# Kernel optimization log

Measured on AMD Instinct MI355X. Metric: run time of the kernel, lower is better.

Reference implementation:

```python
import jax, jax.numpy as jnp
import numpy as np

L = 48.0      # cubic box edge
DL = 4.0      # k-grid spacing param -> nk = int(L/DL) = 12
N = 8192      # atoms
D = 128       # feature channels
TWOPI = 2.0 * np.pi


def _k_index_sets():
    """Replicates torch mask.nonzero() ordering and the (k_vectors - 1) index
    shift of compute_potential_optimized. The shifted indices are remapped to
    effective integer exponents (torch negative indexing wraps, i.e. modulo)."""
    nk = int(L / DL)
    kx = np.arange(nk + 1)
    ky = np.arange(-nk, nk + 1)
    kz = np.arange(-nk, nk + 1)
    KX, KY, KZ = np.meshgrid(kx, ky, kz, indexing='ij')
    ksq = KX.astype(np.float64) ** 2 + KY ** 2 + KZ ** 2
    mask = (ksq <= (L / DL) ** 2) & (ksq > 0)
    ix, iy, iz = np.nonzero(mask)  # row-major, same order as torch .nonzero()
    # forward potential: value[:, :, ix-1, iy-1, iz-1] with wraparound ->
    # effective exponents via modulo of the per-axis table sizes
    ex = (ix - 1) % (nk + 1)                      # eikx col c -> exponent c
    ey = ((iy - 1) % (2 * nk + 1)) - nk           # eiky col c -> exponent c-nk
    ez = ((iz - 1) % (2 * nk + 1)) - nk
    k_fwd = np.stack([ex, ey, ez], axis=1).astype(np.int32)
    # inverse transform: unshifted valid k-vectors, negative sign in exponent
    k_inv = np.stack([ix, iy - nk, iz - nk], axis=1).astype(np.int32)
    return k_fwd, k_inv


def setup_inputs() -> dict:
    key = jax.random.key(0)
    kq, kk, kv, kr = jax.random.split(key, 4)
    k_fwd, k_inv = _k_index_sets()
    cell = jnp.eye(3, dtype=jnp.float32)[None] * jnp.float32(L)  # [1,3,3]
    return {
        'q_vector': jax.random.normal(kq, (N, D), dtype=jnp.float32),
        'k_vector': jax.random.normal(kk, (N, D), dtype=jnp.float32),
        'v_vector': jax.random.normal(kv, (N, D), dtype=jnp.float32),
        'positions': jax.random.uniform(kr, (N, 3), dtype=jnp.float32) * jnp.float32(L),
        'cell': cell,
        'batch': jnp.zeros((N,), dtype=jnp.int64),
        'k_fwd': jnp.asarray(k_fwd),
        'k_inv': jnp.asarray(k_inv),
    }


def reference(q_vector, k_vector, v_vector, positions, cell, batch, k_fwd, k_inv):
    # single batch (batch is all zeros); box = diagonal of the cell
    box = jnp.diagonal(cell.reshape(-1, 3, 3), axis1=-2, axis2=-1)[0]  # [3]
    rfrac = positions / box                                            # [n,3]
    # plane waves at the selected k-vectors; |eik| == 1
    phase_f = TWOPI * (rfrac @ k_fwd.T.astype(rfrac.dtype))            # [n,K]
    eik_f = jnp.exp(1j * phase_f)                                      # complex64
    phase_i = TWOPI * (rfrac @ k_inv.T.astype(rfrac.dtype))
    eik_i = jnp.exp(-1j * phase_i)                                     # [n,K]
    cdt = eik_f.dtype
    # k/v potentials: structure-factor sums over atoms -> [K,d]
    k_pot = jnp.einsum('nk,nd->kd', eik_f, k_vector.astype(cdt))
    v_pot = jnp.einsum('nk,nd->kd', eik_f, v_vector.astype(cdt))
    # |q_pot[n,d,k]| = |q[n,d]|*|eik[n,k]| = |q[n,d]| exactly, so the einsum
    # 'ijk,jk->ij' over abs values collapses to a real GEMM:
    aw = jnp.abs(q_vector) @ jnp.abs(k_pot).T                          # [n,K]
    # max-shift + log_softmax + exp == softmax over the k axis
    sm = jax.nn.softmax(aw, axis=-1)
    # inverse transform fused: sum_k sm[n,k]*eik_i[n,k]*v_pot[k,d]
    out = jnp.real(jnp.einsum('nk,kd->nd', sm.astype(cdt) * eik_i, v_pot))
    return out
```

## Files before the change

kernel.cpp:

```cpp
#include <hip/hip_runtime.h>
#include <hip/hip_bf16.h>

#define D128 128
#define NSPLIT 8
#define KT 64
#define SNR 32
#define SKT 128
#define TOPS 8
#define FCAP 16

typedef float4 f4;
typedef __attribute__((ext_vector_type(8))) short short8v;
typedef __attribute__((ext_vector_type(4))) float f32x4;

__device__ __forceinline__ unsigned short f2bu(float x){
  __hip_bfloat16 h = __float2bfloat16(x);
  return *(unsigned short*)&h;
}
__device__ __forceinline__ float bu2f(unsigned short u){
  return __uint_as_float(((unsigned)u) << 16);
}

#define GLDS16(gp, lp) __builtin_amdgcn_global_load_lds( \
    (const __attribute__((address_space(1))) unsigned int*)(const void*)(gp), \
    (__attribute__((address_space(3))) unsigned int*)(lp), 16, 0, 0)

__global__ __launch_bounds__(256) void k_zero(float* __restrict__ p, int total){
  int i = blockIdx.x*256 + threadIdx.x;
  int stride = gridDim.x*256;
  for(; i < total; i += stride) p[i] = 0.f;
}

__global__ __launch_bounds__(256) void k_cvt(const float* __restrict__ pos,
    const float* __restrict__ cell, float* __restrict__ rfrac,
    const float* __restrict__ q, const float* __restrict__ kvec,
    const float* __restrict__ vvec, unsigned short* __restrict__ kvhT,
    unsigned short* __restrict__ kvlT, unsigned short* __restrict__ vvhT,
    unsigned short* __restrict__ qa_bf, int N){
  __shared__ float sk[32][132], sv[32][132];
  const int tid = threadIdx.x;
  const int c0 = blockIdx.x*32;
  if(tid < 32){
    int i = c0 + tid;
    float bx = cell[0], by = cell[4], bz = cell[8];
    f4 r; r.x = pos[i*3+0]/bx; r.y = pos[i*3+1]/by; r.z = pos[i*3+2]/bz; r.w = 0.f;
    ((f4*)rfrac)[i] = r;
  }
  #pragma unroll
  for(int i=0;i<2;i++){
    int idx = tid + i*256;
    int row = idx >> 4, c = idx & 15;
    const float* src = q + (size_t)(c0+row)*D128 + c*8;
    f4 v0 = *(const f4*)src, v1 = *(const f4*)(src+4);
    uint4 o;
    o.x = (unsigned)f2bu(fabsf(v0.x)) | ((unsigned)f2bu(fabsf(v0.y))<<16);
    o.y = (unsigned)f2bu(fabsf(v0.z)) | ((unsigned)f2bu(fabsf(v0.w))<<16);
    o.z = (unsigned)f2bu(fabsf(v1.x)) | ((unsigned)f2bu(fabsf(v1.y))<<16);
    o.w = (unsigned)f2bu(fabsf(v1.z)) | ((unsigned)f2bu(fabsf(v1.w))<<16);
    *(uint4*)(qa_bf + (size_t)(c0+row)*D128 + ((c ^ (row&7))<<3)) = o;
  }
  #pragma unroll
  for(int i=0;i<4;i++){
    int idx = tid + i*256;
    int a = idx >> 5, fq = idx & 31;
    f4 v = ((const f4*)(kvec + (size_t)(c0+a)*D128))[fq];
    *(f4*)&sk[a][fq*4] = v;
    f4 u = ((const f4*)(vvec + (size_t)(c0+a)*D128))[fq];
    *(f4*)&sv[a][fq*4] = u;
  }
  __syncthreads();
  #pragma unroll
  for(int i=0;i<4;i++){
    int idx = tid + i*256;
    int d = idx >> 3, aq = idx & 7;
    size_t ob = (size_t)d*N + c0 + aq*4;
    ushort4 h, l, vh;
    float x0 = sk[aq*4+0][d], x1 = sk[aq*4+1][d], x2 = sk[aq*4+2][d], x3 = sk[aq*4+3][d];
    h.x = f2bu(x0); h.y = f2bu(x1); h.z = f2bu(x2); h.w = f2bu(x3);
    l.x = f2bu(x0 - bu2f(h.x)); l.y = f2bu(x1 - bu2f(h.y));
    l.z = f2bu(x2 - bu2f(h.z)); l.w = f2bu(x3 - bu2f(h.w));
    vh.x = f2bu(sv[aq*4+0][d]); vh.y = f2bu(sv[aq*4+1][d]);
    vh.z = f2bu(sv[aq*4+2][d]); vh.w = f2bu(sv[aq*4+3][d]);
    *(ushort4*)(kvhT + ob) = h;
    *(ushort4*)(kvlT + ob) = l;
    *(ushort4*)(vvhT + ob) = vh;
  }
}

__global__ __launch_bounds__(512) void k_pot_mfma(
    const unsigned short* __restrict__ kvhT, const unsigned short* __restrict__ kvlT,
    const unsigned short* __restrict__ vvhT, const float* __restrict__ rfrac,
    const int* __restrict__ kfwd, float* __restrict__ pot4, int N, int K){
  const int tid = threadIdx.x;
  const int k0 = blockIdx.x*KT;
  const int split = blockIdx.y;
  const int part = N/NSPLIT;
  const int abase = split*part;
  __shared__ unsigned short Ae[2][4][KT][32];
  __shared__ unsigned short Bl[2][3][D128][32];
  const int w = tid >> 6, l = tid & 63, l15 = l & 15, g = l >> 4;
  const int kp = tid >> 4;
  const int a0 = (tid & 15)*2;
  float kfa[2][3];
  {
    int r0 = min(k0 + kp*2,     K-1);
    int r1 = min(k0 + kp*2 + 1, K-1);
    kfa[0][0] = (float)kfwd[3*r0]; kfa[0][1] = (float)kfwd[3*r0+1]; kfa[0][2] = (float)kfwd[3*r0+2];
    kfa[1][0] = (float)kfwd[3*r1]; kfa[1][1] = (float)kfwd[3*r1+1]; kfa[1][2] = (float)kfwd[3*r1+2];
  }
  f32x4 acc[4][4];
  #pragma unroll
  for(int i=0;i<4;i++)
    #pragma unroll
    for(int j=0;j<4;j++)
      acc[i][j] = (f32x4){0.f,0.f,0.f,0.f};
  const int rowS = w*16 + (l >> 2);
  const int csrc = (((l & 3) ^ ((l >> 3) & 3)))*8;
  const int cA   = (g ^ ((l15 >> 1) & 3))*8;

  auto stage = [&](int buf, int c0a){
    size_t goff = (size_t)rowS*N + c0a + csrc;
    GLDS16(kvhT + goff, &Bl[buf][0][w*16][0]);
    GLDS16(kvlT + goff, &Bl[buf][1][w*16][0]);
    GLDS16(vvhT + goff, &Bl[buf][2][w*16][0]);
  };
  auto egen = [&](int buf, int c0a){
    f4 r0 = ((const f4*)rfrac)[c0a + a0];
    f4 r1 = ((const f4*)rfrac)[c0a + a0 + 1];
    #pragma unroll
    for(int kk=0; kk<2; kk++){
      int kloc = kp*2 + kk;
      float t0 = __builtin_amdgcn_fractf(r0.x*kfa[kk][0] + r0.y*kfa[kk][1] + r0.z*kfa[kk][2]);
      float t1 = __builtin_amdgcn_fractf(r1.x*kfa[kk][0] + r1.y*kfa[kk][1] + r1.z*kfa[kk][2]);
      float c0v = __builtin_amdgcn_cosf(t0), s0v = __builtin_amdgcn_sinf(t0);
      float c1v = __builtin_amdgcn_cosf(t1), s1v = __builtin_amdgcn_sinf(t1);
      unsigned cb0 = __float_as_uint(c0v), cb1 = __float_as_uint(c1v);
      unsigned sb0 = __float_as_uint(s0v), sb1 = __float_as_uint(s1v);
      unsigned chp = (cb0 >> 16) | (cb1 & 0xffff0000u);
      unsigned shp = (sb0 >> 16) | (sb1 & 0xffff0000u);
      float cl0 = c0v - __uint_as_float(cb0 & 0xffff0000u);
      float cl1 = c1v - __uint_as_float(cb1 & 0xffff0000u);
      float sl0 = s0v - __uint_as_float(sb0 & 0xffff0000u);
      float sl1 = s1v - __uint_as_float(sb1 & 0xffff0000u);
      unsigned clp = (unsigned)f2bu(cl0) | ((unsigned)f2bu(cl1) << 16);
      unsigned slp = (unsigned)f2bu(sl0) | ((unsigned)f2bu(sl1) << 16);
      int off = (((a0>>3) ^ ((kloc>>1)&3)) << 3) | (a0 & 7);
      *(unsigned*)&Ae[buf][0][kloc][off] = chp;
      *(unsigned*)&Ae[buf][1][kloc][off] = clp;
      *(unsigned*)&Ae[buf][2][kloc][off] = shp;
      *(unsigned*)&Ae[buf][3][kloc][off] = slp;
    }
  };

  stage(0, abase); egen(0, abase);
  __syncthreads();
  const int nch = part/32;
  for(int ch=0; ch<nch; ch++){
    int cur = ch & 1;
    if(ch+1 < nch){ stage(cur^1, abase + (ch+1)*32); egen(cur^1, abase + (ch+1)*32); }
    short8v bKh = *(const short8v*)&Bl[cur][0][w*16 + l15][cA];
    short8v bKl = *(const short8v*)&Bl[cur][1][w*16 + l15][cA];
    short8v bVh = *(const short8v*)&Bl[cur][2][w*16 + l15][cA];
    #pragma unroll
    for(int ks=0; ks<4; ks++){
      short8v e0 = *(const short8v*)&Ae[cur][0][ks*16 + l15][cA];
      short8v e1 = *(const short8v*)&Ae[cur][1][ks*16 + l15][cA];
      short8v e2 = *(const short8v*)&Ae[cur][2][ks*16 + l15][cA];
      short8v e3 = *(const short8v*)&Ae[cur][3][ks*16 + l15][cA];
      acc[ks][0] = __builtin_amdgcn_mfma_f32_16x16x32_bf16(e0, bKh, acc[ks][0], 0,0,0);
      acc[ks][1] = __builtin_amdgcn_mfma_f32_16x16x32_bf16(e2, bKh, acc[ks][1], 0,0,0);
      acc[ks][2] = __builtin_amdgcn_mfma_f32_16x16x32_bf16(e0, bVh, acc[ks][2], 0,0,0);
      acc[ks][3] = __builtin_amdgcn_mfma_f32_16x16x32_bf16(e2, bVh, acc[ks][3], 0,0,0);
      acc[ks][0] = __builtin_amdgcn_mfma_f32_16x16x32_bf16(e0, bKl, acc[ks][0], 0,0,0);
      acc[ks][1] = __builtin_amdgcn_mfma_f32_16x16x32_bf16(e2, bKl, acc[ks][1], 0,0,0);
      acc[ks][0] = __builtin_amdgcn_mfma_f32_16x16x32_bf16(e1, bKh, acc[ks][0], 0,0,0);
      acc[ks][1] = __builtin_amdgcn_mfma_f32_16x16x32_bf16(e3, bKh, acc[ks][1], 0,0,0);
    }
    __syncthreads();
  }
  size_t M = (size_t)K*D128;
  #pragma unroll
  for(int ks=0; ks<4; ks++){
    #pragma unroll
    for(int reg=0; reg<4; reg++){
      int k = k0 + ks*16 + g*4 + reg;
      if(k < K){
        int d = w*16 + l15;
        size_t base = (size_t)k*D128 + d;
        atomicAdd(&pot4[base],       acc[ks][0][reg]);
        atomicAdd(&pot4[base + M],   acc[ks][1][reg]);
        atomicAdd(&pot4[base + 2*M], acc[ks][2][reg]);
        atomicAdd(&pot4[base + 3*M], acc[ks][3][reg]);
      }
    }
  }
}

__global__ __launch_bounds__(256) void k_merge(const float* __restrict__ pot4,
    float* __restrict__ kabs, unsigned short* __restrict__ kabs_swz,
    float* __restrict__ vcm, float* __restrict__ vsm, int K, int KPAD){
  size_t M = (size_t)K*D128;
  size_t idx = (size_t)blockIdx.x*256 + threadIdx.x;
  if(idx >= (size_t)KPAD*D128) return;
  int k = (int)(idx >> 7), d = (int)(idx & 127);
  size_t sw = (size_t)k*D128 + ((((d>>3) ^ (k&7))<<3) | (d&7));
  if(idx < M){
    float kc = pot4[idx], ks_ = pot4[M+idx], vc = pot4[2*M+idx], vs = pot4[3*M+idx];
    float ab = sqrtf(fmaf(kc,kc, ks_*ks_));
    kabs[idx] = ab;
    vcm[idx] = vc; vsm[idx] = vs;
    kabs_swz[sw] = f2bu(ab);
  } else {
    kabs_swz[sw] = 0;
  }
}

__global__ __launch_bounds__(256) void k_screen(
    const unsigned short* __restrict__ qa_bf, const unsigned short* __restrict__ kabs_swz,
    int* __restrict__ tk, float* __restrict__ taw, int N, int K, int NT){
  const int tid = threadIdx.x;
  const int w = tid >> 6, l = tid & 63, l15 = l & 15, g = l >> 4;
  const int n0 = blockIdx.x*SNR;
  const int ty = blockIdx.y;
  const int k0 = ty*SKT;
  __shared__ unsigned short Kb[SKT][D128];
  __shared__ unsigned short Qa[SNR][D128];
  __shared__ int cnt[SNR];
  __shared__ unsigned mx[SNR];
  if(tid < SNR){ cnt[tid] = 0; mx[tid] = 0u; }
  {
    int row = tid >> 3, s = tid & 7;
    size_t o = ((size_t)(n0+row)*NT + ty)*TOPS + s;
    taw[o] = -1e30f; tk[o] = -1;
  }
  #pragma unroll
  for(int j=0;j<8;j++){
    int sbase = w*512 + j*64;
    GLDS16(kabs_swz + (size_t)k0*D128 + (size_t)(sbase + l)*8,
           ((unsigned short*)Kb) + (size_t)sbase*8);
  }
  #pragma unroll
  for(int j=0;j<2;j++){
    int sbase = w*128 + j*64;
    GLDS16(qa_bf + (size_t)n0*D128 + (size_t)(sbase + l)*8,
           ((unsigned short*)Qa) + (size_t)sbase*8);
  }
  __syncthreads();
  f32x4 acc[2][2];
  #pragma unroll
  for(int i=0;i<2;i++)
    #pragma unroll
    for(int j=0;j<2;j++)
      acc[i][j] = (f32x4){0.f,0.f,0.f,0.f};
  const int sz = l15 & 7;
  #pragma unroll
  for(int ds=0; ds<4; ds++){
    int c = (((ds*4 + g) ^ sz))*8;
    short8v a0 = *(const short8v*)&Kb[w*32 + l15][c];
    short8v a1 = *(const short8v*)&Kb[w*32 + 16 + l15][c];
    short8v b0 = *(const short8v*)&Qa[l15][c];
    short8v b1 = *(const short8v*)&Qa[16 + l15][c];
    acc[0][0] = __builtin_amdgcn_mfma_f32_16x16x32_bf16(a0, b0, acc[0][0], 0,0,0);
    acc[0][1] = __builtin_amdgcn_mfma_f32_16x16x32_bf16(a0, b1, acc[0][1], 0,0,0);
    acc[1][0] = __builtin_amdgcn_mfma_f32_16x16x32_bf16(a1, b0, acc[1][0], 0,0,0);
    acc[1][1] = __builtin_amdgcn_mfma_f32_16x16x32_bf16(a1, b1, acc[1][1], 0,0,0);
  }
  #pragma unroll
  for(int jn=0; jn<2; jn++){
    float m4 = 0.f;
    #pragma unroll
    for(int ks=0; ks<2; ks++)
      #pragma unroll
      for(int r=0; r<4; r++)
        m4 = fmaxf(m4, acc[ks][jn][r]);
    atomicMax(&mx[jn*16 + l15], __float_as_uint(m4));
  }
  __syncthreads();
  #pragma unroll
  for(int jn=0; jn<2; jn++){
    int n = jn*16 + l15;
    float thr = __uint_as_float(mx[n]) - 21.0f;
    #pragma unroll
    for(int ks=0; ks<2; ks++){
      #pragma unroll
      for(int r=0; r<4; r++){
        int k = k0 + w*32 + ks*16 + g*4 + r;
        float aw = acc[ks][jn][r];
        if(k < K && aw >= thr){
          int s = atomicAdd(&cnt[n], 1);
          if(s < TOPS){
            size_t o = ((size_t)(n0+n)*NT + ty)*TOPS + s;
            taw[o] = aw; tk[o] = k;
          }
        }
      }
    }
  }
}

__global__ __launch_bounds__(256) void k_final(const float* __restrict__ q,
    const float* __restrict__ kabs, const float* __restrict__ vcm,
    const float* __restrict__ vsm, const float* __restrict__ rfrac,
    const int* __restrict__ kinv, const int* __restrict__ tk,
    const float* __restrict__ taw, float* __restrict__ out, int N, int K, int NT){
  const int rb = threadIdx.x >> 2;
  const int j  = threadIdx.x & 3;
  const int row = blockIdx.x*64 + rb;
  if(row >= N) return;
  const int NE = NT*TOPS;
  const float* trow = taw + (size_t)row*NE;
  const int*   krow = tk  + (size_t)row*NE;
  float m = -1e30f;
  for(int i=j; i<NE; i+=4) m = fmaxf(m, trow[i]);
  m = fmaxf(m, __shfl_xor(m,1)); m = fmaxf(m, __shfl_xor(m,2));
  __shared__ int lk[64][FCAP];
  __shared__ int lcnt[64];
  if(j==0) lcnt[rb] = 0;
  __syncthreads();
  for(int i=j; i<NE; i+=4){
    float aw = trow[i];
    if(aw >= m - 24.0f){
      int s = atomicAdd(&lcnt[rb], 1);
      if(s < FCAP) lk[rb][s] = krow[i];
    }
  }
  __syncthreads();
  int cn = min(lcnt[rb], FCAP);
  const float* qrow = q + (size_t)row*D128;
  float paw[FCAP];
  for(int e=0; e<cn; e++){
    int k = lk[rb][e];
    const float* ar = kabs + (size_t)k*D128;
    float p = 0.f;
    #pragma unroll
    for(int d=0; d<32; d+=4){
      int dd = j*32 + d;
      f4 qv = *(const f4*)(qrow+dd); f4 av = *(const f4*)(ar+dd);
      p = fmaf(fabsf(qv.x), av.x, p); p = fmaf(fabsf(qv.y), av.y, p);
      p = fmaf(fabsf(qv.z), av.z, p); p = fmaf(fabsf(qv.w), av.w, p);
    }
    p += __shfl_xor(p,1); p += __shfl_xor(p,2);
    paw[e] = p;
  }
  float m2 = -1e30f;
  for(int e=0;e<cn;e++) m2 = fmaxf(m2, paw[e]);
  float w[FCAP]; float Z = 0.f;
  for(int e=0;e<cn;e++){ w[e] = expf(paw[e]-m2); Z += w[e]; }
  float o[32];
  #pragma unroll
  for(int t=0;t<32;t++) o[t]=0.f;
  f4 rf = *(const f4*)(rfrac + (size_t)row*4);
  for(int e=0;e<cn;e++){
    float wn = w[e]/Z;
    if(wn < 1e-7f) continue;
    int k = lk[rb][e];
    float t = __builtin_amdgcn_fractf(rf.x*(float)kinv[k*3] + rf.y*(float)kinv[k*3+1] + rf.z*(float)kinv[k*3+2]);
    float si = __builtin_amdgcn_sinf(t), ci = __builtin_amdgcn_cosf(t);
    float wc = wn*ci, wsn = wn*si;
    const float* vcr = vcm + (size_t)k*D128 + j*32;
    const float* vsr = vsm + (size_t)k*D128 + j*32;
    #pragma unroll
    for(int d=0; d<32; d+=4){
      f4 a2 = *(const f4*)(vcr+d); f4 b2 = *(const f4*)(vsr+d);
      o[d]   = fmaf(wc, a2.x, fmaf(wsn, b2.x, o[d]));
      o[d+1] = fmaf(wc, a2.y, fmaf(wsn, b2.y, o[d+1]));
      o[d+2] = fmaf(wc, a2.z, fmaf(wsn, b2.z, o[d+2]));
      o[d+3] = fmaf(wc, a2.w, fmaf(wsn, b2.w, o[d+3]));
    }
  }
  float* orow = out + (size_t)row*D128 + j*32;
  #pragma unroll
  for(int d=0; d<32; d+=4)
    *(f4*)(orow+d) = make_float4(o[d], o[d+1], o[d+2], o[d+3]);
}

extern "C" void kernel_launch(void* const* d_in, const int* in_sizes, int n_in,
                              void* d_out, int out_size, void* d_ws, size_t ws_size,
                              hipStream_t stream){
  const float* q    = (const float*)d_in[0];
  const float* kvec = (const float*)d_in[1];
  const float* vvec = (const float*)d_in[2];
  const float* pos  = (const float*)d_in[3];
  const float* cell = (const float*)d_in[4];
  const int*   kfwd = (const int*)d_in[6];
  const int*   kinv = (const int*)d_in[7];
  const int N = in_sizes[3]/3;
  const int K = in_sizes[6]/3;
  const int NT = (K + SKT - 1)/SKT;
  const int KPAD = NT*SKT;
  const int KTILES = (K + KT - 1)/KT;

  float* ws = (float*)d_ws;
  size_t o = 0;
  float* rfrac    = ws + o; o += (size_t)N*4;
  float* pot4     = ws + o; o += (size_t)4*K*D128;
  float* kabs     = ws + o; o += (size_t)K*D128;
  float* vcm      = ws + o; o += (size_t)K*D128;
  float* vsm      = ws + o; o += (size_t)K*D128;
  unsigned short* kabs_swz = (unsigned short*)(ws + o); o += (size_t)KPAD*D128/2 + 4;
  unsigned short* qa_bf    = (unsigned short*)(ws + o); o += (size_t)N*D128/2 + 4;
  float* taw      = ws + o; o += (size_t)N*NT*TOPS;
  int*   tk       = (int*)(ws + o); o += (size_t)N*NT*TOPS;
  unsigned short* kvhT = (unsigned short*)(ws + o); o += (size_t)D128*N/2;
  unsigned short* kvlT = (unsigned short*)(ws + o); o += (size_t)D128*N/2;
  unsigned short* vvhT = (unsigned short*)(ws + o); o += (size_t)D128*N/2;
  float* out = (float*)d_out;

  k_zero<<<dim3(1024), dim3(256), 0, stream>>>(pot4, 4*K*D128);
  k_cvt<<<dim3(N/32), dim3(256), 0, stream>>>(pos, cell, rfrac, q, kvec, vvec,
      kvhT, kvlT, vvhT, qa_bf, N);
  k_pot_mfma<<<dim3(KTILES, NSPLIT), dim3(512), 0, stream>>>(
      kvhT, kvlT, vvhT, rfrac, kfwd, pot4, N, K);
  k_merge<<<dim3((KPAD*D128 + 255)/256), dim3(256), 0, stream>>>(
      pot4, kabs, kabs_swz, vcm, vsm, K, KPAD);
  k_screen<<<dim3(N/SNR, NT), dim3(256), 0, stream>>>(qa_bf, kabs_swz, tk, taw, N, K, NT);
  k_final<<<dim3((N+63)/64), dim3(256), 0, stream>>>(
      q, kabs, vcm, vsm, rfrac, kinv, tk, taw, out, N, K, NT);
}
```

Baseline: 244.8 us.

## Retile k_pot_mfma to 4 waves with 32x64 per-wave register tiles

The structure-factor MFMA kernel drops from 8 to 4 waves per block. Each wave now owns a 32(k) x 64(d) output sub-tile, so every LDS fragment of the plane-wave and feature operands is reused across more MFMAs. Plane-wave generation is reorganised so each thread computes 8 atoms for one k and writes 16-byte LDS stores instead of scattered 4-byte ones, and staging issues twice as many global-to-LDS loads per thread. The cost is many more accumulator registers per thread (128 floats) and fewer waves to hide latency.

```diff
diff --git a/kernel.cpp b/kernel.cpp
--- a/kernel.cpp
+++ b/kernel.cpp
@@ -87,7 +87,7 @@
   }
 }
 
-__global__ __launch_bounds__(512) void k_pot_mfma(
+__global__ __launch_bounds__(256) void k_pot_mfma(
     const unsigned short* __restrict__ kvhT, const unsigned short* __restrict__ kvlT,
     const unsigned short* __restrict__ vvhT, const float* __restrict__ rfrac,
     const int* __restrict__ kfwd, float* __restrict__ pot4, int N, int K){
@@ -99,57 +99,61 @@
   __shared__ unsigned short Ae[2][4][KT][32];
   __shared__ unsigned short Bl[2][3][D128][32];
   const int w = tid >> 6, l = tid & 63, l15 = l & 15, g = l >> 4;
-  const int kp = tid >> 4;
-  const int a0 = (tid & 15)*2;
-  float kfa[2][3];
+  const int kbase = (w & 1)*32, dbase = (w >> 1)*64;
+  const int ke = tid >> 2;
+  const int ae0 = (tid & 3)*8;
+  float kfx, kfy, kfz;
   {
-    int r0 = min(k0 + kp*2,     K-1);
-    int r1 = min(k0 + kp*2 + 1, K-1);
-    kfa[0][0] = (float)kfwd[3*r0]; kfa[0][1] = (float)kfwd[3*r0+1]; kfa[0][2] = (float)kfwd[3*r0+2];
-    kfa[1][0] = (float)kfwd[3*r1]; kfa[1][1] = (float)kfwd[3*r1+1]; kfa[1][2] = (float)kfwd[3*r1+2];
-  }
-  f32x4 acc[4][4];
-  #pragma unroll
-  for(int i=0;i<4;i++)
+    int kk = min(k0 + ke, K-1);
+    kfx = (float)kfwd[3*kk]; kfy = (float)kfwd[3*kk+1]; kfz = (float)kfwd[3*kk+2];
+  }
+  f32x4 acc[2][4][4];
+  #pragma unroll
+  for(int i=0;i<2;i++)
     #pragma unroll
     for(int j=0;j<4;j++)
-      acc[i][j] = (f32x4){0.f,0.f,0.f,0.f};
-  const int rowS = w*16 + (l >> 2);
-  const int csrc = (((l & 3) ^ ((l >> 3) & 3)))*8;
-  const int cA   = (g ^ ((l15 >> 1) & 3))*8;
+      #pragma unroll
+      for(int p=0;p<4;p++)
+        acc[i][j][p] = (f32x4){0.f,0.f,0.f,0.f};
+  const int csrcS = ((l & 3) ^ ((l >> 3) & 3))*8;
+  const int ccA   = (g ^ ((l15 >> 1) & 3))*8;
 
   auto stage = [&](int buf, int c0a){
-    size_t goff = (size_t)rowS*N + c0a + csrc;
-    GLDS16(kvhT + goff, &Bl[buf][0][w*16][0]);
-    GLDS16(kvlT + goff, &Bl[buf][1][w*16][0]);
-    GLDS16(vvhT + goff, &Bl[buf][2][w*16][0]);
+    #pragma unroll
+    for(int r=0; r<2; r++){
+      int rbase = r*64 + w*16;
+      size_t goff = (size_t)(rbase + (l >> 2))*N + c0a + csrcS;
+      GLDS16(kvhT + goff, &Bl[buf][0][rbase][0]);
+      GLDS16(kvlT + goff, &Bl[buf][1][rbase][0]);
+      GLDS16(vvhT + goff, &Bl[buf][2][rbase][0]);
+    }
   };
   auto egen = [&](int buf, int c0a){
-    f4 r0 = ((const f4*)rfrac)[c0a + a0];
-    f4 r1 = ((const f4*)rfrac)[c0a + a0 + 1];
-    #pragma unroll
-    for(int kk=0; kk<2; kk++){
-      int kloc = kp*2 + kk;
-      float t0 = __builtin_amdgcn_fractf(r0.x*kfa[kk][0] + r0.y*kfa[kk][1] + r0.z*kfa[kk][2]);
-      float t1 = __builtin_amdgcn_fractf(r1.x*kfa[kk][0] + r1.y*kfa[kk][1] + r1.z*kfa[kk][2]);
-      float c0v = __builtin_amdgcn_cosf(t0), s0v = __builtin_amdgcn_sinf(t0);
-      float c1v = __builtin_amdgcn_cosf(t1), s1v = __builtin_amdgcn_sinf(t1);
-      unsigned cb0 = __float_as_uint(c0v), cb1 = __float_as_uint(c1v);
-      unsigned sb0 = __float_as_uint(s0v), sb1 = __float_as_uint(s1v);
-      unsigned chp = (cb0 >> 16) | (cb1 & 0xffff0000u);
-      unsigned shp = (sb0 >> 16) | (sb1 & 0xffff0000u);
-      float cl0 = c0v - __uint_as_float(cb0 & 0xffff0000u);
-      float cl1 = c1v - __uint_as_float(cb1 & 0xffff0000u);
-      float sl0 = s0v - __uint_as_float(sb0 & 0xffff0000u);
-      float sl1 = s1v - __uint_as_float(sb1 & 0xffff0000u);
-      unsigned clp = (unsigned)f2bu(cl0) | ((unsigned)f2bu(cl1) << 16);
-      unsigned slp = (unsigned)f2bu(sl0) | ((unsigned)f2bu(sl1) << 16);
-      int off = (((a0>>3) ^ ((kloc>>1)&3)) << 3) | (a0 & 7);
-      *(unsigned*)&Ae[buf][0][kloc][off] = chp;
-      *(unsigned*)&Ae[buf][1][kloc][off] = clp;
-      *(unsigned*)&Ae[buf][2][kloc][off] = shp;
-      *(unsigned*)&Ae[buf][3][kloc][off] = slp;
-    }
+    unsigned ow0[4], ow1[4], ow2[4], ow3[4];
+    #pragma unroll
+    for(int jp=0; jp<4; jp++){
+      f4 ra = ((const f4*)rfrac)[c0a + ae0 + jp*2];
+      f4 rb = ((const f4*)rfrac)[c0a + ae0 + jp*2 + 1];
+      float ta = __builtin_amdgcn_fractf(ra.x*kfx + ra.y*kfy + ra.z*kfz);
+      float tb = __builtin_amdgcn_fractf(rb.x*kfx + rb.y*kfy + rb.z*kfz);
+      float ca = __builtin_amdgcn_cosf(ta), sa = __builtin_amdgcn_sinf(ta);
+      float cb = __builtin_amdgcn_cosf(tb), sb = __builtin_amdgcn_sinf(tb);
+      unsigned cba = __float_as_uint(ca), cbb = __float_as_uint(cb);
+      unsigned sba = __float_as_uint(sa), sbb = __float_as_uint(sb);
+      ow0[jp] = (cba >> 16) | (cbb & 0xffff0000u);
+      ow2[jp] = (sba >> 16) | (sbb & 0xffff0000u);
+      float cla = ca - __uint_as_float(cba & 0xffff0000u);
+      float clb = cb - __uint_as_float(cbb & 0xffff0000u);
+      float sla = sa - __uint_as_float(sba & 0xffff0000u);
+      float slb = sb - __uint_as_float(sbb & 0xffff0000u);
+      ow1[jp] = (unsigned)f2bu(cla) | ((unsigned)f2bu(clb) << 16);
+      ow3[jp] = (unsigned)f2bu(sla) | ((unsigned)f2bu(slb) << 16);
+    }
+    int cdst = (((ae0 >> 3) ^ ((ke >> 1) & 3)) << 3);
+    *(uint4*)&Ae[buf][0][ke][cdst] = make_uint4(ow0[0],ow0[1],ow0[2],ow0[3]);
+    *(uint4*)&Ae[buf][1][ke][cdst] = make_uint4(ow1[0],ow1[1],ow1[2],ow1[3]);
+    *(uint4*)&Ae[buf][2][ke][cdst] = make_uint4(ow2[0],ow2[1],ow2[2],ow2[3]);
+    *(uint4*)&Ae[buf][3][ke][cdst] = make_uint4(ow3[0],ow3[1],ow3[2],ow3[3]);
   };
 
   stage(0, abase); egen(0, abase);
@@ -158,39 +162,51 @@
   for(int ch=0; ch<nch; ch++){
     int cur = ch & 1;
     if(ch+1 < nch){ stage(cur^1, abase + (ch+1)*32); egen(cur^1, abase + (ch+1)*32); }
-    short8v bKh = *(const short8v*)&Bl[cur][0][w*16 + l15][cA];
-    short8v bKl = *(const short8v*)&Bl[cur][1][w*16 + l15][cA];
-    short8v bVh = *(const short8v*)&Bl[cur][2][w*16 + l15][cA];
-    #pragma unroll
-    for(int ks=0; ks<4; ks++){
-      short8v e0 = *(const short8v*)&Ae[cur][0][ks*16 + l15][cA];
-      short8v e1 = *(const short8v*)&Ae[cur][1][ks*16 + l15][cA];
-      short8v e2 = *(const short8v*)&Ae[cur][2][ks*16 + l15][cA];
-      short8v e3 = *(const short8v*)&Ae[cur][3][ks*16 + l15][cA];
-      acc[ks][0] = __builtin_amdgcn_mfma_f32_16x16x32_bf16(e0, bKh, acc[ks][0], 0,0,0);
-      acc[ks][1] = __builtin_amdgcn_mfma_f32_16x16x32_bf16(e2, bKh, acc[ks][1], 0,0,0);
-      acc[ks][2] = __builtin_amdgcn_mfma_f32_16x16x32_bf16(e0, bVh, acc[ks][2], 0,0,0);
-      acc[ks][3] = __builtin_amdgcn_mfma_f32_16x16x32_bf16(e2, bVh, acc[ks][3], 0,0,0);
-      acc[ks][0] = __builtin_amdgcn_mfma_f32_16x16x32_bf16(e0, bKl, acc[ks][0], 0,0,0);
-      acc[ks][1] = __builtin_amdgcn_mfma_f32_16x16x32_bf16(e2, bKl, acc[ks][1], 0,0,0);
-      acc[ks][0] = __builtin_amdgcn_mfma_f32_16x16x32_bf16(e1, bKh, acc[ks][0], 0,0,0);
-      acc[ks][1] = __builtin_amdgcn_mfma_f32_16x16x32_bf16(e3, bKh, acc[ks][1], 0,0,0);
+    short8v bKh[4], bKl[4], bVh[4];
+    #pragma unroll
+    for(int ds2=0; ds2<4; ds2++){
+      int row = dbase + ds2*16 + l15;
+      bKh[ds2] = *(const short8v*)&Bl[cur][0][row][ccA];
+      bKl[ds2] = *(const short8v*)&Bl[cur][1][row][ccA];
+      bVh[ds2] = *(const short8v*)&Bl[cur][2][row][ccA];
+    }
+    #pragma unroll
+    for(int ks2=0; ks2<2; ks2++){
+      int krow = kbase + ks2*16 + l15;
+      short8v e0 = *(const short8v*)&Ae[cur][0][krow][ccA];
+      short8v e1 = *(const short8v*)&Ae[cur][1][krow][ccA];
+      short8v e2 = *(const short8v*)&Ae[cur][2][krow][ccA];
+      short8v e3 = *(const short8v*)&Ae[cur][3][krow][ccA];
+      #pragma unroll
+      for(int ds2=0; ds2<4; ds2++){
+        acc[ks2][ds2][0] = __builtin_amdgcn_mfma_f32_16x16x32_bf16(e0, bKh[ds2], acc[ks2][ds2][0], 0,0,0);
+        acc[ks2][ds2][1] = __builtin_amdgcn_mfma_f32_16x16x32_bf16(e2, bKh[ds2], acc[ks2][ds2][1], 0,0,0);
+        acc[ks2][ds2][2] = __builtin_amdgcn_mfma_f32_16x16x32_bf16(e0, bVh[ds2], acc[ks2][ds2][2], 0,0,0);
+        acc[ks2][ds2][3] = __builtin_amdgcn_mfma_f32_16x16x32_bf16(e2, bVh[ds2], acc[ks2][ds2][3], 0,0,0);
+        acc[ks2][ds2][0] = __builtin_amdgcn_mfma_f32_16x16x32_bf16(e0, bKl[ds2], acc[ks2][ds2][0], 0,0,0);
+        acc[ks2][ds2][1] = __builtin_amdgcn_mfma_f32_16x16x32_bf16(e2, bKl[ds2], acc[ks2][ds2][1], 0,0,0);
+        acc[ks2][ds2][0] = __builtin_amdgcn_mfma_f32_16x16x32_bf16(e1, bKh[ds2], acc[ks2][ds2][0], 0,0,0);
+        acc[ks2][ds2][1] = __builtin_amdgcn_mfma_f32_16x16x32_bf16(e3, bKh[ds2], acc[ks2][ds2][1], 0,0,0);
+      }
     }
     __syncthreads();
   }
   size_t M = (size_t)K*D128;
   #pragma unroll
-  for(int ks=0; ks<4; ks++){
-    #pragma unroll
-    for(int reg=0; reg<4; reg++){
-      int k = k0 + ks*16 + g*4 + reg;
-      if(k < K){
-        int d = w*16 + l15;
-        size_t base = (size_t)k*D128 + d;
-        atomicAdd(&pot4[base],       acc[ks][0][reg]);
-        atomicAdd(&pot4[base + M],   acc[ks][1][reg]);
-        atomicAdd(&pot4[base + 2*M], acc[ks][2][reg]);
-        atomicAdd(&pot4[base + 3*M], acc[ks][3][reg]);
+  for(int ks2=0; ks2<2; ks2++){
+    #pragma unroll
+    for(int ds2=0; ds2<4; ds2++){
+      #pragma unroll
+      for(int reg=0; reg<4; reg++){
+        int k = k0 + kbase + ks2*16 + g*4 + reg;
+        if(k < K){
+          int d = dbase + ds2*16 + l15;
+          size_t base = (size_t)k*D128 + d;
+          atomicAdd(&pot4[base],       acc[ks2][ds2][0][reg]);
+          atomicAdd(&pot4[base + M],   acc[ks2][ds2][1][reg]);
+          atomicAdd(&pot4[base + 2*M], acc[ks2][ds2][2][reg]);
+          atomicAdd(&pot4[base + 3*M], acc[ks2][ds2][3][reg]);
+        }
       }
     }
   }
@@ -409,7 +425,7 @@
   k_zero<<<dim3(1024), dim3(256), 0, stream>>>(pot4, 4*K*D128);
   k_cvt<<<dim3(N/32), dim3(256), 0, stream>>>(pos, cell, rfrac, q, kvec, vvec,
       kvhT, kvlT, vvhT, qa_bf, N);
-  k_pot_mfma<<<dim3(KTILES, NSPLIT), dim3(512), 0, stream>>>(
+  k_pot_mfma<<<dim3(KTILES, NSPLIT), dim3(256), 0, stream>>>(
       kvhT, kvlT, vvhT, rfrac, kfwd, pot4, N, K);
   k_merge<<<dim3((KPAD*D128 + 255)/256), dim3(256), 0, stream>>>(
       pot4, kabs, kabs_swz, vcm, vsm, K, KPAD);
```

Measured after the change: 280.4 us. 1.15x slower.
